# Optimization experiments

Hardware: AMD Instinct MI355X
Metric: run time of the kernel (lower is better)

Reference implementation:

```python
import jax, jax.numpy as jnp
import numpy as np

B, C, H, W = 4, 512, 128, 128
C8 = C // 8


def setup_inputs() -> dict:
    key = jax.random.key(0)
    ks = jax.random.split(key, 10)
    s = 0.02
    return {
        "x_exmplar": jax.random.normal(ks[0], (B, C, H, W), jnp.float32),
        "x_query": jax.random.normal(ks[1], (B, C, H, W), jnp.float32),
        "Wq": jax.random.normal(ks[2], (C8, C), jnp.float32) * s,
        "bq": jax.random.normal(ks[3], (C8,), jnp.float32) * s,
        "Wk": jax.random.normal(ks[4], (C8, C), jnp.float32) * s,
        "bk": jax.random.normal(ks[5], (C8,), jnp.float32) * s,
        "Wv": jax.random.normal(ks[6], (C, C), jnp.float32) * s,
        "bv": jax.random.normal(ks[7], (C,), jnp.float32) * s,
        "gamma_1": jax.random.normal(ks[8], (1,), jnp.float32) * 0.1,
        "gamma_2": jax.random.normal(ks[9], (1,), jnp.float32) * 0.1,
    }


def _conv1x1(x, Wt, b):
    # x: (B,C,H,W), Wt: (O,C) -> (B,O,H,W)
    return jnp.einsum('bchw,oc->bohw', x, Wt) + b[None, :, None, None]


def reference(x_exmplar, x_query, Wq, bq, Wk, bk, Wv, bv, gamma_1, gamma_2):
    q = _conv1x1(x_query, Wq, bq)      # (B,C8,H,W)
    k = _conv1x1(x_exmplar, Wk, bk)    # (B,C8,H,W)
    v = _conv1x1(x_exmplar, Wv, bv)    # (B,C,H,W)

    # vertical (H) path: energy_H[b,h,w,j] = sum_c q[b,c,h,w] k[b,c,j,w], -inf on h==j
    energy_H = jnp.einsum('bchw,bcjw->bhwj', q, k)
    eye = jnp.eye(H, dtype=bool)[None, :, None, :]       # (1,H,1,H)
    energy_H = jnp.where(eye, -jnp.inf, energy_H)
    # horizontal (W) path: energy_W[b,h,w,j] = sum_c q[b,c,h,w] k[b,c,h,j]
    energy_W = jnp.einsum('bchw,bchj->bhwj', q, k)

    concate = jax.nn.softmax(jnp.concatenate([energy_H, energy_W], axis=-1), axis=-1)
    att_H = concate[..., :H]           # (B,H,W,H)
    att_W = concate[..., H:]           # (B,H,W,W)

    out_H = jnp.einsum('bcjw,bhwj->bchw', v, att_H)
    out_W = jnp.einsum('bchj,bhwj->bchw', v, att_W)

    # diagonal (LR / RL) paths; D = min(H,W) = H for square maps
    q_d = jnp.diagonal(q, axis1=2, axis2=3)   # (B,C8,D)
    k_d = jnp.diagonal(k, axis1=2, axis2=3)   # (B,C8,D)
    v_d = jnp.diagonal(v, axis1=2, axis2=3)   # (B,C,D)
    # diag of transpose(2,3) with offset 0 equals diag, so LR == RL faithfully
    energy_LR = jnp.einsum('bci,bcj->bij', k_d, q_d)  # (B,D,D)
    energy_RL = energy_LR
    # softmax over a singleton trailing axis (as in the original code)
    out_LR = jax.nn.softmax(jnp.einsum('bcd,bdj->bcj', v_d, energy_LR)[..., None], axis=3)
    out_RL = jax.nn.softmax(jnp.einsum('bcd,bdj->bcj', v_d, energy_RL)[..., None], axis=3)

    out_sum = out_H + out_W + out_LR + out_RL   # (B,C,H,W) via broadcast of (B,C,D,1)
    return (gamma_1 * out_sum + x_exmplar, gamma_2 * out_sum + x_query)
```

## Files before the change

kernel.cpp:

```cpp
#include <hip/hip_runtime.h>
#include <stdint.h>

typedef unsigned short u16;
typedef __attribute__((ext_vector_type(8))) short bf16x8;
typedef __attribute__((ext_vector_type(4))) float f32x4;

#define NB   4
#define NC   512
#define NC8  64
#define NH   128
#define NW   128
#define NHW  16384

__device__ __forceinline__ float b2f(u16 u) {
  union { float f; uint32_t i; } x; x.i = ((uint32_t)u) << 16; return x.f;
}
__device__ __forceinline__ u16 f2b(float f) {
  union { float f; uint32_t u; } x; x.f = f;
  uint32_t r = x.u + 0x7FFF + ((x.u >> 16) & 1);
  return (u16)(r >> 16);
}
__device__ __forceinline__ uint4 pack8bf(const float* f) {
  uint4 u;
  u.x = (uint32_t)f2b(f[0]) | ((uint32_t)f2b(f[1]) << 16);
  u.y = (uint32_t)f2b(f[2]) | ((uint32_t)f2b(f[3]) << 16);
  u.z = (uint32_t)f2b(f[4]) | ((uint32_t)f2b(f[5]) << 16);
  u.w = (uint32_t)f2b(f[6]) | ((uint32_t)f2b(f[7]) << 16);
  return u;
}
__device__ __forceinline__ void unpack8bf(uint4 u, float* f) {
  f[0] = b2f((u16)(u.x & 0xFFFF)); f[1] = b2f((u16)(u.x >> 16));
  f[2] = b2f((u16)(u.y & 0xFFFF)); f[3] = b2f((u16)(u.y >> 16));
  f[4] = b2f((u16)(u.z & 0xFFFF)); f[5] = b2f((u16)(u.z >> 16));
  f[6] = b2f((u16)(u.w & 0xFFFF)); f[7] = b2f((u16)(u.w >> 16));
}

__global__ __launch_bounds__(256) void convert_w3(const float* __restrict__ Wv,
                                                  const float* __restrict__ Wq,
                                                  const float* __restrict__ Wk,
                                                  u16* __restrict__ wv,
                                                  u16* __restrict__ wq,
                                                  u16* __restrict__ wk) {
  int bid = blockIdx.x;
  const float* W; u16* Wb; int base;
  if (bid < 128)      { W = Wv; Wb = wv; base = bid; }
  else if (bid < 144) { W = Wq; Wb = wq; base = bid - 128; }
  else                { W = Wk; Wb = wk; base = bid - 144; }
  int i = (base * 256 + threadIdx.x) * 8;
  float4 a = *reinterpret_cast<const float4*>(W + i);
  float4 b = *reinterpret_cast<const float4*>(W + i + 4);
  float f[8] = {a.x, a.y, a.z, a.w, b.x, b.y, b.z, b.w};
  *reinterpret_cast<uint4*>(Wb + i) = pack8bf(f);
}

__global__ __launch_bounds__(256) void transpose_cvt2(const float* __restrict__ xe,
                                                      const float* __restrict__ xq,
                                                      u16* __restrict__ xeT,
                                                      u16* __restrict__ xqT) {
  __shared__ float tile[64][68];
  int z = blockIdx.z;
  int b = z & 3;
  const float* x = (z < 4) ? xe : xq;
  u16* xT = (z < 4) ? xeT : xqT;
  int c0 = blockIdx.y * 64, n0 = blockIdx.x * 64;
  int t = threadIdx.x;
  const float* src = x + ((size_t)b * NC + c0) * NHW + n0;
  int r = t >> 2, cq = (t & 3) * 16;
#pragma unroll
  for (int v = 0; v < 4; v++) {
    float4 f = *reinterpret_cast<const float4*>(&src[(size_t)r * NHW + cq + v * 4]);
    *reinterpret_cast<float4*>(&tile[r][cq + v * 4]) = f;
  }
  __syncthreads();
  int n = t >> 2, cg = (t & 3) * 16;
  u16* dst = &xT[((size_t)b * NHW + n0 + n) * NC + c0 + cg];
#pragma unroll
  for (int half = 0; half < 2; half++) {
    float f[8];
#pragma unroll
    for (int j = 0; j < 8; j++) f[j] = tile[cg + half * 8 + j][n];
    *reinterpret_cast<uint4*>(dst + half * 8) = pack8bf(f);
  }
}

__global__ __launch_bounds__(256) void proj64_qk(const u16* __restrict__ xeT,
                                                 const u16* __restrict__ xqT,
                                                 const u16* __restrict__ wk,
                                                 const u16* __restrict__ wq,
                                                 const float* __restrict__ bk,
                                                 const float* __restrict__ bq,
                                                 u16* __restrict__ kT,
                                                 u16* __restrict__ qT) {
  __shared__ __align__(16) u16 smem[12288];
  char* AsB = (char*)smem;
  char* BsB = (char*)smem + 8192;
  int which = blockIdx.y;
  const u16* xT = which ? xqT : xeT;
  const u16* Wb = which ? wq : wk;
  const float* bias = which ? bq : bk;
  u16* yT = which ? qT : kT;
  int n0 = blockIdx.x * 128, b = blockIdx.z;
  int t = threadIdx.x;
  int wid = t >> 6, lane = t & 63;
  int wm = wid >> 1, wn = wid & 1;
  int l15 = lane & 15, lhi = lane >> 4;

  f32x4 acc[2][4];
#pragma unroll
  for (int m = 0; m < 2; m++)
#pragma unroll
    for (int n = 0; n < 4; n++)
#pragma unroll
      for (int r = 0; r < 4; r++) acc[m][n][r] = 0.f;

  const u16* Bbase = xT + ((size_t)b * NHW + n0) * NC;

  for (int c0 = 0; c0 < NC; c0 += 64) {
#pragma unroll
    for (int p = 0; p < 2; p++) {
      int idx = t + p * 256;
      int row = idx >> 3, cb = (idx & 7) * 8;
      int dst = row * 128 + ((cb * 2) ^ ((row & 7) << 4));
      bf16x8 av = *reinterpret_cast<const bf16x8*>(Wb + (size_t)row * NC + c0 + cb);
      *reinterpret_cast<bf16x8*>(AsB + dst) = av;
    }
#pragma unroll
    for (int p = 0; p < 4; p++) {
      int idx = t + p * 256;
      int row = idx >> 3, cb = (idx & 7) * 8;
      int dst = row * 128 + ((cb * 2) ^ ((row & 7) << 4));
      bf16x8 bv = *reinterpret_cast<const bf16x8*>(Bbase + (size_t)row * NC + c0 + cb);
      *reinterpret_cast<bf16x8*>(BsB + dst) = bv;
    }
    __syncthreads();
#pragma unroll
    for (int kk = 0; kk < 2; kk++) {
      int kbyte = kk * 64 + lhi * 16;
      bf16x8 af[2], bfr[4];
#pragma unroll
      for (int m = 0; m < 2; m++) {
        int row = wm * 32 + m * 16 + l15;
        af[m] = *reinterpret_cast<const bf16x8*>(AsB + row * 128 + (kbyte ^ ((row & 7) << 4)));
      }
#pragma unroll
      for (int n = 0; n < 4; n++) {
        int row = wn * 64 + n * 16 + l15;
        bfr[n] = *reinterpret_cast<const bf16x8*>(BsB + row * 128 + (kbyte ^ ((row & 7) << 4)));
      }
#pragma unroll
      for (int m = 0; m < 2; m++)
#pragma unroll
        for (int n = 0; n < 4; n++)
          acc[m][n] = __builtin_amdgcn_mfma_f32_16x16x32_bf16(af[m], bfr[n], acc[m][n], 0, 0, 0);
    }
    __syncthreads();
  }

  char* stage = (char*)smem;
#pragma unroll
  for (int m = 0; m < 2; m++) {
#pragma unroll
    for (int r = 0; r < 4; r++) {
      int o = wm * 32 + m * 16 + lhi * 4 + r;
      float bval = bias[o];
#pragma unroll
      for (int n = 0; n < 4; n++) {
        int col = wn * 64 + n * 16 + l15;
        int byte = col * 128 + ((o * 2) ^ ((col & 7) << 4));
        *reinterpret_cast<u16*>(stage + byte) = f2b(acc[m][n][r] + bval);
      }
    }
  }
  __syncthreads();
#pragma unroll
  for (int p = 0; p < 4; p++) {
    int idx = t + p * 256;
    int col = idx >> 3, seg = idx & 7;
    int byte = col * 128 + ((seg * 16) ^ ((col & 7) << 4));
    uint4 v = *reinterpret_cast<const uint4*>(stage + byte);
    *reinterpret_cast<uint4*>(&yT[((size_t)b * NHW + n0 + col) * 64 + seg * 8]) = v;
  }
}

__global__ __launch_bounds__(256) void proj_v_mfma(const u16* __restrict__ xT,
                                                   const u16* __restrict__ Wb,
                                                   const float* __restrict__ bias,
                                                   u16* __restrict__ y) {
  __shared__ __align__(16) u16 smem[16384];
  char* AsB = (char*)smem;
  char* BsB = (char*)(smem + 8192);
  int o0 = blockIdx.x * 128, n0 = blockIdx.y * 128, b = blockIdx.z;
  int t = threadIdx.x;
  int wid = t >> 6, lane = t & 63;
  int wm = wid >> 1, wn = wid & 1;
  int l15 = lane & 15, lhi = lane >> 4;

  f32x4 acc[4][4];
#pragma unroll
  for (int m = 0; m < 4; m++)
#pragma unroll
    for (int n = 0; n < 4; n++)
#pragma unroll
      for (int r = 0; r < 4; r++) acc[m][n][r] = 0.f;

  const u16* Arow = Wb + (size_t)o0 * NC;
  const u16* Brow = xT + ((size_t)b * NHW + n0) * NC;

  for (int c0 = 0; c0 < NC; c0 += 64) {
#pragma unroll
    for (int p = 0; p < 4; p++) {
      int idx = t + p * 256;
      int row = idx >> 3;
      int cb  = (idx & 7) * 8;
      int dst = row * 128 + ((cb * 2) ^ ((row & 7) << 4));
      bf16x8 av = *reinterpret_cast<const bf16x8*>(Arow + (size_t)row * NC + c0 + cb);
      *reinterpret_cast<bf16x8*>(AsB + dst) = av;
      bf16x8 bv = *reinterpret_cast<const bf16x8*>(Brow + (size_t)row * NC + c0 + cb);
      *reinterpret_cast<bf16x8*>(BsB + dst) = bv;
    }
    __syncthreads();
#pragma unroll
    for (int kk = 0; kk < 2; kk++) {
      int kbyte = kk * 64 + lhi * 16;
      bf16x8 af[4], bfr[4];
#pragma unroll
      for (int m = 0; m < 4; m++) {
        int row = wm * 64 + m * 16 + l15;
        af[m] = *reinterpret_cast<const bf16x8*>(AsB + row * 128 + (kbyte ^ ((row & 7) << 4)));
      }
#pragma unroll
      for (int n = 0; n < 4; n++) {
        int row = wn * 64 + n * 16 + l15;
        bfr[n] = *reinterpret_cast<const bf16x8*>(BsB + row * 128 + (kbyte ^ ((row & 7) << 4)));
      }
#pragma unroll
      for (int m = 0; m < 4; m++)
#pragma unroll
        for (int n = 0; n < 4; n++)
          acc[m][n] = __builtin_amdgcn_mfma_f32_16x16x32_bf16(af[m], bfr[n], acc[m][n], 0, 0, 0);
    }
    __syncthreads();
  }

  char* stage = (char*)smem + wid * 8192;
#pragma unroll
  for (int m = 0; m < 4; m++) {
#pragma unroll
    for (int r = 0; r < 4; r++) {
      int lrow = m * 16 + lhi * 4 + r;
      float bval = bias[o0 + wm * 64 + lrow];
#pragma unroll
      for (int n = 0; n < 4; n++) {
        int col = n * 16 + l15;
        *reinterpret_cast<u16*>(stage + lrow * 128 + col * 2) = f2b(acc[m][n][r] + bval);
      }
    }
  }
  __syncthreads();
#pragma unroll
  for (int s = 0; s < 8; s++) {
    int row  = s * 8 + (lane >> 3);
    int colb = (lane & 7) * 8;
    uint4 v = *reinterpret_cast<const uint4*>(stage + row * 128 + colb * 2);
    size_t addr = ((size_t)b * NC + o0 + wm * 64 + row) * (size_t)NHW + n0 + wn * 64 + colb;
    *reinterpret_cast<uint4*>(&y[addr]) = v;
  }
}

__global__ __launch_bounds__(256) void transpose128v(const u16* __restrict__ src,
                                                     u16* __restrict__ dst) {
  __shared__ u16 tile[64][68];
  int p = blockIdx.z;
  int i0 = blockIdx.y * 64, j0 = blockIdx.x * 64;
  int t = threadIdx.x;
  const u16* s = src + (size_t)p * NHW;
  u16* d = dst + (size_t)p * NHW;
#pragma unroll
  for (int q = 0; q < 2; q++) {
    int idx = t + q * 256;
    int r = idx >> 3, c8 = (idx & 7) * 8;
    uint4 v = *reinterpret_cast<const uint4*>(&s[(size_t)(i0 + r) * 128 + j0 + c8]);
    *reinterpret_cast<uint2*>(&tile[r][c8])     = make_uint2(v.x, v.y);
    *reinterpret_cast<uint2*>(&tile[r][c8 + 4]) = make_uint2(v.z, v.w);
  }
  __syncthreads();
#pragma unroll
  for (int q = 0; q < 2; q++) {
    int idx = t + q * 256;
    int j = idx >> 3, c8 = (idx & 7) * 8;
    u16 f[8];
#pragma unroll
    for (int v = 0; v < 8; v++) f[v] = tile[c8 + v][j];
    uint4 o;
    o.x = (uint32_t)f[0] | ((uint32_t)f[1] << 16);
    o.y = (uint32_t)f[2] | ((uint32_t)f[3] << 16);
    o.z = (uint32_t)f[4] | ((uint32_t)f[5] << 16);
    o.w = (uint32_t)f[6] | ((uint32_t)f[7] << 16);
    *reinterpret_cast<uint4*>(&d[(size_t)(j0 + j) * 128 + i0 + c8]) = o;
  }
}

__global__ __launch_bounds__(256) void energy2(const u16* __restrict__ QT,
                                               const u16* __restrict__ KT,
                                               u16* __restrict__ att) {
  __shared__ __align__(16) u16 smem[16384];
  char* AsB = (char*)smem;
  char* BsB = (char*)(smem + 8192);
  int s = blockIdx.x, b = blockIdx.y, isH = blockIdx.z;
  int t = threadIdx.x;
  int wid = t >> 6, lane = t & 63;
  int wm = wid >> 1, wn = wid & 1;
  int l15 = lane & 15, lhi = lane >> 4;

  size_t base = (size_t)b * NHW * 64;
  size_t rowstride = isH ? (size_t)128 * 64 : 64;
  size_t off0 = isH ? (size_t)s * 64 : (size_t)s * 128 * 64;

  f32x4 acc[4][4];
#pragma unroll
  for (int m = 0; m < 4; m++)
#pragma unroll
    for (int n = 0; n < 4; n++)
#pragma unroll
      for (int r = 0; r < 4; r++) acc[m][n][r] = 0.f;

#pragma unroll
  for (int p = 0; p < 4; p++) {
    int idx = t + p * 256;
    int row = idx >> 3;
    int cb  = (idx & 7) * 8;
    int dst = row * 128 + ((cb * 2) ^ ((row & 7) << 4));
    bf16x8 av = *reinterpret_cast<const bf16x8*>(QT + base + off0 + (size_t)row * rowstride + cb);
    *reinterpret_cast<bf16x8*>(AsB + dst) = av;
    bf16x8 bv = *reinterpret_cast<const bf16x8*>(KT + base + off0 + (size_t)row * rowstride + cb);
    *reinterpret_cast<bf16x8*>(BsB + dst) = bv;
  }
  __syncthreads();
#pragma unroll
  for (int kk = 0; kk < 2; kk++) {
    int kbyte = kk * 64 + lhi * 16;
    bf16x8 af[4], bfr[4];
#pragma unroll
    for (int m = 0; m < 4; m++) {
      int row = wm * 64 + m * 16 + l15;
      af[m] = *reinterpret_cast<const bf16x8*>(AsB + row * 128 + (kbyte ^ ((row & 7) << 4)));
    }
#pragma unroll
    for (int n = 0; n < 4; n++) {
      int row = wn * 64 + n * 16 + l15;
      bfr[n] = *reinterpret_cast<const bf16x8*>(BsB + row * 128 + (kbyte ^ ((row & 7) << 4)));
    }
#pragma unroll
    for (int m = 0; m < 4; m++)
#pragma unroll
      for (int n = 0; n < 4; n++)
        acc[m][n] = __builtin_amdgcn_mfma_f32_16x16x32_bf16(af[m], bfr[n], acc[m][n], 0, 0, 0);
  }
  __syncthreads();

  char* stage = (char*)smem + wid * 8192;
#pragma unroll
  for (int m = 0; m < 4; m++) {
#pragma unroll
    for (int r = 0; r < 4; r++) {
      int lrow = m * 16 + lhi * 4 + r;
      int grow = wm * 64 + lrow;
#pragma unroll
      for (int n = 0; n < 4; n++) {
        int col = n * 16 + l15;
        int gcol = wn * 64 + col;
        float v = acc[m][n][r];
        if (isH && gcol == grow) v = -1e30f;
        *reinterpret_cast<u16*>(stage + lrow * 128 + col * 2) = f2b(v);
      }
    }
  }
  __syncthreads();
  size_t attb = (size_t)b * 4194304;
#pragma unroll
  for (int sb = 0; sb < 8; sb++) {
    int row  = wm * 64 + sb * 8 + (lane >> 3);
    int colb = wn * 64 + (lane & 7) * 8;
    uint4 v = *reinterpret_cast<const uint4*>(stage + (sb * 8 + (lane >> 3)) * 128 + (lane & 7) * 16);
    size_t addr = attb + (isH ? ((size_t)row * 32768 + (size_t)s * 256 + colb)
                              : ((size_t)s * 32768 + (size_t)row * 256 + 128 + colb));
    *reinterpret_cast<uint4*>(&att[addr]) = v;
  }
}

__global__ __launch_bounds__(256) void softmax_kern(u16* __restrict__ att) {
  int half = threadIdx.x >> 5;
  int lane = threadIdx.x & 31;
  size_t row = (size_t)blockIdx.x * 8 + half;
  u16* p = att + row * 256;
  uint4 u = *reinterpret_cast<const uint4*>(&p[lane * 8]);
  float v[8]; unpack8bf(u, v);
  float mx = v[0];
  for (int i = 1; i < 8; i++) mx = fmaxf(mx, v[i]);
  for (int off = 16; off; off >>= 1) mx = fmaxf(mx, __shfl_xor(mx, off));
  float sum = 0.f;
  for (int i = 0; i < 8; i++) { v[i] = __expf(v[i] - mx); sum += v[i]; }
  for (int off = 16; off; off >>= 1) sum += __shfl_xor(sum, off);
  float inv = 1.f / sum;
  for (int i = 0; i < 8; i++) v[i] *= inv;
  *reinterpret_cast<uint4*>(&p[lane * 8]) = pack8bf(v);
}

__global__ __launch_bounds__(256) void out_gemm2(const u16* __restrict__ Vn,
                                                 const u16* __restrict__ Vsw,
                                                 const u16* __restrict__ att) {
  __shared__ __align__(16) u16 smem[16384];
  char* AsB = (char*)smem;
  char* BsB = (char*)(smem + 8192);
  int ct = blockIdx.x, s = blockIdx.y;
  int b = blockIdx.z & 3, isH = blockIdx.z >> 2;
  const u16* V = isH ? Vsw : Vn;
  u16* out = const_cast<u16*>(V);
  int t = threadIdx.x;
  int wid = t >> 6, lane = t & 63;
  int wm = wid >> 1, wn = wid & 1;
  int l15 = lane & 15, lhi = lane >> 4;

  f32x4 acc[4][4];
#pragma unroll
  for (int m = 0; m < 4; m++)
#pragma unroll
    for (int n = 0; n < 4; n++)
#pragma unroll
      for (int r = 0; r < 4; r++) acc[m][n][r] = 0.f;

  const u16* Abase = V + ((size_t)(b * NC + ct * 128)) * NHW + (size_t)s * 128;
  size_t attb = (size_t)b * 4194304;
  size_t bbase = attb + (isH ? (size_t)s * 256 : (size_t)s * 32768 + 128);
  size_t bstride = isH ? 32768 : 256;

  for (int c0 = 0; c0 < 128; c0 += 64) {
#pragma unroll
    for (int p = 0; p < 4; p++) {
      int idx = t + p * 256;
      int row = idx >> 3;
      int cb  = (idx & 7) * 8;
      int dst = row * 128 + ((cb * 2) ^ ((row & 7) << 4));
      bf16x8 av = *reinterpret_cast<const bf16x8*>(Abase + (size_t)row * NHW + c0 + cb);
      *reinterpret_cast<bf16x8*>(AsB + dst) = av;
      bf16x8 bv = *reinterpret_cast<const bf16x8*>(att + bbase + (size_t)row * bstride + c0 + cb);
      *reinterpret_cast<bf16x8*>(BsB + dst) = bv;
    }
    __syncthreads();
#pragma unroll
    for (int kk = 0; kk < 2; kk++) {
      int kbyte = kk * 64 + lhi * 16;
      bf16x8 af[4], bfr[4];
#pragma unroll
      for (int m = 0; m < 4; m++) {
        int row = wm * 64 + m * 16 + l15;
        af[m] = *reinterpret_cast<const bf16x8*>(AsB + row * 128 + (kbyte ^ ((row & 7) << 4)));
      }
#pragma unroll
      for (int n = 0; n < 4; n++) {
        int row = wn * 64 + n * 16 + l15;
        bfr[n] = *reinterpret_cast<const bf16x8*>(BsB + row * 128 + (kbyte ^ ((row & 7) << 4)));
      }
#pragma unroll
      for (int m = 0; m < 4; m++)
#pragma unroll
        for (int n = 0; n < 4; n++)
          acc[m][n] = __builtin_amdgcn_mfma_f32_16x16x32_bf16(af[m], bfr[n], acc[m][n], 0, 0, 0);
    }
    __syncthreads();
  }

  char* stage = (char*)smem + wid * 8192;
#pragma unroll
  for (int m = 0; m < 4; m++) {
#pragma unroll
    for (int r = 0; r < 4; r++) {
      int lrow = m * 16 + lhi * 4 + r;
#pragma unroll
      for (int n = 0; n < 4; n++) {
        int col = n * 16 + l15;
        *reinterpret_cast<u16*>(stage + lrow * 128 + col * 2) = f2b(acc[m][n][r]);
      }
    }
  }
  __syncthreads();
#pragma unroll
  for (int sb = 0; sb < 8; sb++) {
    int row  = sb * 8 + (lane >> 3);
    int colb = (lane & 7) * 8;
    uint4 v = *reinterpret_cast<const uint4*>(stage + row * 128 + colb * 2);
    size_t addr = ((size_t)(b * NC + ct * 128 + wm * 64 + row)) * NHW + (size_t)s * 128 + wn * 64 + colb;
    *reinterpret_cast<uint4*>(&out[addr]) = v;
  }
}

__global__ __launch_bounds__(256) void epilogue(const u16* __restrict__ outWbf,
                                                const u16* __restrict__ outHsw,
                                                const float* __restrict__ xe,
                                                const float* __restrict__ xq,
                                                const float* __restrict__ g1p,
                                                const float* __restrict__ g2p,
                                                float* __restrict__ out0,
                                                float* __restrict__ out1) {
  __shared__ float tile[32][65];
  int p = blockIdx.z;
  int h0 = blockIdx.y * 64, w0 = blockIdx.x * 32;
  int t = threadIdx.x;
  {
    int w = t >> 3, hc = t & 7;
    uint4 v = *reinterpret_cast<const uint4*>(
        &outHsw[(size_t)p * NHW + (size_t)(w0 + w) * 128 + h0 + hc * 8]);
    float f[8]; unpack8bf(v, f);
    for (int j = 0; j < 8; j++) tile[w][hc * 8 + j] = f[j];
  }
  __syncthreads();
  float g1 = g1p[0], g2 = g2p[0];
  int h = t >> 2, wc = t & 3;
  size_t idx = (size_t)p * NHW + (size_t)(h0 + h) * 128 + w0 + wc * 8;
  uint4 wv = *reinterpret_cast<const uint4*>(&outWbf[idx]);
  float s[8]; unpack8bf(wv, s);
  float4 xe0 = *reinterpret_cast<const float4*>(&xe[idx]);
  float4 xe1 = *reinterpret_cast<const float4*>(&xe[idx + 4]);
  float4 xq0 = *reinterpret_cast<const float4*>(&xq[idx]);
  float4 xq1 = *reinterpret_cast<const float4*>(&xq[idx + 4]);
  float sum[8];
  for (int j = 0; j < 8; j++) sum[j] = s[j] + tile[wc * 8 + j][h] + 2.0f;
  float4 o0a = {g1 * sum[0] + xe0.x, g1 * sum[1] + xe0.y, g1 * sum[2] + xe0.z, g1 * sum[3] + xe0.w};
  float4 o0b = {g1 * sum[4] + xe1.x, g1 * sum[5] + xe1.y, g1 * sum[6] + xe1.z, g1 * sum[7] + xe1.w};
  float4 o1a = {g2 * sum[0] + xq0.x, g2 * sum[1] + xq0.y, g2 * sum[2] + xq0.z, g2 * sum[3] + xq0.w};
  float4 o1b = {g2 * sum[4] + xq1.x, g2 * sum[5] + xq1.y, g2 * sum[6] + xq1.z, g2 * sum[7] + xq1.w};
  *reinterpret_cast<float4*>(&out0[idx])     = o0a;
  *reinterpret_cast<float4*>(&out0[idx + 4]) = o0b;
  *reinterpret_cast<float4*>(&out1[idx])     = o1a;
  *reinterpret_cast<float4*>(&out1[idx + 4]) = o1b;
}

extern "C" void kernel_launch(void* const* d_in, const int* in_sizes, int n_in,
                              void* d_out, int out_size, void* d_ws, size_t ws_size,
                              hipStream_t stream) {
  (void)in_sizes; (void)n_in; (void)out_size; (void)ws_size;
  const float* xe = (const float*)d_in[0];
  const float* xq = (const float*)d_in[1];
  const float* Wq = (const float*)d_in[2];
  const float* bq = (const float*)d_in[3];
  const float* Wk = (const float*)d_in[4];
  const float* bk = (const float*)d_in[5];
  const float* Wv = (const float*)d_in[6];
  const float* bv = (const float*)d_in[7];
  const float* g1 = (const float*)d_in[8];
  const float* g2 = (const float*)d_in[9];
  float* out = (float*)d_out;

  char* ws = (char*)d_ws;
  u16* qT    = (u16*)(ws + 0);
  u16* kT    = (u16*)(ws + 8388608);
  u16* wv_bf = (u16*)(ws + 16777216);
  u16* wq_bf = (u16*)(ws + 17301504);
  u16* wk_bf = (u16*)(ws + 17367040);
  u16* v_n   = (u16*)(ws + 33554432);
  u16* v_sw  = (u16*)(ws + 100663296);
  u16* att   = (u16*)(ws + 167772160);
  u16* xeT   = (u16*)(ws + 201326592);
  u16* xqT   = (u16*)(ws + 100663296);

  convert_w3<<<dim3(160), 256, 0, stream>>>(Wv, Wq, Wk, wv_bf, wq_bf, wk_bf);
  transpose_cvt2<<<dim3(256, 8, 8), 256, 0, stream>>>(xe, xq, xeT, xqT);
  proj64_qk<<<dim3(128, 2, 4), 256, 0, stream>>>(xeT, xqT, wk_bf, wq_bf, bk, bq, kT, qT);
  proj_v_mfma<<<dim3(4, 128, 4), 256, 0, stream>>>(xeT, wv_bf, bv, v_n);
  transpose128v<<<dim3(2, 2, 2048), 256, 0, stream>>>(v_n, v_sw);
  energy2<<<dim3(128, 4, 2), 256, 0, stream>>>(qT, kT, att);
  softmax_kern<<<dim3(8192), 256, 0, stream>>>(att);
  out_gemm2<<<dim3(4, 128, 8), 256, 0, stream>>>(v_n, v_sw, att);
  epilogue<<<dim3(4, 2, 2048), 256, 0, stream>>>(v_n, v_sw, xe, xq, g1, g2,
                                                 out, out + 33554432);
}
```

Before: 748.2 us.

## Register-prefetch next K tile in GEMMs, remap block order, fold weight conversion

The three MFMA GEMM kernels (q/k projection, v projection, output GEMM) now load the next K-slice of the global tiles into registers while the current slice is being consumed, so global latency overlaps with MFMA work. proj_v_mfma and out_gemm2 remap the linear block index with a stride-8 swizzle, which changes the order in which tiles are dispatched and may improve cache locality across chiplets. The weight bf16 conversion is folded into the transpose kernel as an extra z-slice to save one launch. The cost is higher register pressure from the prefetch buffers, plus many mostly idle blocks in the extra z-slice.

```diff
diff --git a/kernel.cpp b/kernel.cpp
--- a/kernel.cpp
+++ b/kernel.cpp
@@ -35,30 +35,32 @@
   f[6] = b2f((u16)(u.w & 0xFFFF)); f[7] = b2f((u16)(u.w >> 16));
 }
 
-__global__ __launch_bounds__(256) void convert_w3(const float* __restrict__ Wv,
-                                                  const float* __restrict__ Wq,
-                                                  const float* __restrict__ Wk,
-                                                  u16* __restrict__ wv,
-                                                  u16* __restrict__ wq,
-                                                  u16* __restrict__ wk) {
-  int bid = blockIdx.x;
-  const float* W; u16* Wb; int base;
-  if (bid < 128)      { W = Wv; Wb = wv; base = bid; }
-  else if (bid < 144) { W = Wq; Wb = wq; base = bid - 128; }
-  else                { W = Wk; Wb = wk; base = bid - 144; }
-  int i = (base * 256 + threadIdx.x) * 8;
-  float4 a = *reinterpret_cast<const float4*>(W + i);
-  float4 b = *reinterpret_cast<const float4*>(W + i + 4);
-  float f[8] = {a.x, a.y, a.z, a.w, b.x, b.y, b.z, b.w};
-  *reinterpret_cast<uint4*>(Wb + i) = pack8bf(f);
-}
-
 __global__ __launch_bounds__(256) void transpose_cvt2(const float* __restrict__ xe,
                                                       const float* __restrict__ xq,
                                                       u16* __restrict__ xeT,
-                                                      u16* __restrict__ xqT) {
+                                                      u16* __restrict__ xqT,
+                                                      const float* __restrict__ Wv,
+                                                      const float* __restrict__ Wq,
+                                                      const float* __restrict__ Wk,
+                                                      u16* __restrict__ wv,
+                                                      u16* __restrict__ wq,
+                                                      u16* __restrict__ wk) {
   __shared__ float tile[64][68];
   int z = blockIdx.z;
+  if (z == 8) {
+    int bid = blockIdx.y * 256 + blockIdx.x;
+    if (bid >= 160) return;
+    const float* W; u16* Wb; int base;
+    if (bid < 128)      { W = Wv; Wb = wv; base = bid; }
+    else if (bid < 144) { W = Wq; Wb = wq; base = bid - 128; }
+    else                { W = Wk; Wb = wk; base = bid - 144; }
+    int i = (base * 256 + threadIdx.x) * 8;
+    float4 a = *reinterpret_cast<const float4*>(W + i);
+    float4 b = *reinterpret_cast<const float4*>(W + i + 4);
+    float f[8] = {a.x, a.y, a.z, a.w, b.x, b.y, b.z, b.w};
+    *reinterpret_cast<uint4*>(Wb + i) = pack8bf(f);
+    return;
+  }
   int b = z & 3;
   const float* x = (z < 4) ? xe : xq;
   u16* xT = (z < 4) ? xeT : xqT;
@@ -115,24 +117,51 @@
 
   const u16* Bbase = xT + ((size_t)b * NHW + n0) * NC;
 
-  for (int c0 = 0; c0 < NC; c0 += 64) {
+  bf16x8 ar[2], br[4];
+#pragma unroll
+  for (int p = 0; p < 2; p++) {
+    int idx = t + p * 256;
+    int row = idx >> 3, cb = (idx & 7) * 8;
+    ar[p] = *reinterpret_cast<const bf16x8*>(Wb + (size_t)row * NC + cb);
+  }
+#pragma unroll
+  for (int p = 0; p < 4; p++) {
+    int idx = t + p * 256;
+    int row = idx >> 3, cb = (idx & 7) * 8;
+    br[p] = *reinterpret_cast<const bf16x8*>(Bbase + (size_t)row * NC + cb);
+  }
+
+  for (int tt = 0; tt < 8; tt++) {
 #pragma unroll
     for (int p = 0; p < 2; p++) {
       int idx = t + p * 256;
       int row = idx >> 3, cb = (idx & 7) * 8;
       int dst = row * 128 + ((cb * 2) ^ ((row & 7) << 4));
-      bf16x8 av = *reinterpret_cast<const bf16x8*>(Wb + (size_t)row * NC + c0 + cb);
-      *reinterpret_cast<bf16x8*>(AsB + dst) = av;
+      *reinterpret_cast<bf16x8*>(AsB + dst) = ar[p];
     }
 #pragma unroll
     for (int p = 0; p < 4; p++) {
       int idx = t + p * 256;
       int row = idx >> 3, cb = (idx & 7) * 8;
       int dst = row * 128 + ((cb * 2) ^ ((row & 7) << 4));
-      bf16x8 bv = *reinterpret_cast<const bf16x8*>(Bbase + (size_t)row * NC + c0 + cb);
-      *reinterpret_cast<bf16x8*>(BsB + dst) = bv;
+      *reinterpret_cast<bf16x8*>(BsB + dst) = br[p];
     }
     __syncthreads();
+    if (tt < 7) {
+      int c0 = (tt + 1) * 64;
+#pragma unroll
+      for (int p = 0; p < 2; p++) {
+        int idx = t + p * 256;
+        int row = idx >> 3, cb = (idx & 7) * 8;
+        ar[p] = *reinterpret_cast<const bf16x8*>(Wb + (size_t)row * NC + c0 + cb);
+      }
+#pragma unroll
+      for (int p = 0; p < 4; p++) {
+        int idx = t + p * 256;
+        int row = idx >> 3, cb = (idx & 7) * 8;
+        br[p] = *reinterpret_cast<const bf16x8*>(Bbase + (size_t)row * NC + c0 + cb);
+      }
+    }
 #pragma unroll
     for (int kk = 0; kk < 2; kk++) {
       int kbyte = kk * 64 + lhi * 16;
@@ -189,7 +218,11 @@
   __shared__ __align__(16) u16 smem[16384];
   char* AsB = (char*)smem;
   char* BsB = (char*)(smem + 8192);
-  int o0 = blockIdx.x * 128, n0 = blockIdx.y * 128, b = blockIdx.z;
+  int lin = blockIdx.x + (blockIdx.y << 2) + (blockIdx.z << 9);
+  int l = ((lin & 7) << 8) + (lin >> 3);
+  int o0 = (l & 3) * 128;
+  int n0 = ((l >> 2) & 127) * 128;
+  int b  = l >> 9;
   int t = threadIdx.x;
   int wid = t >> 6, lane = t & 63;
   int wm = wid >> 1, wn = wid & 1;
@@ -206,19 +239,35 @@
   const u16* Arow = Wb + (size_t)o0 * NC;
   const u16* Brow = xT + ((size_t)b * NHW + n0) * NC;
 
-  for (int c0 = 0; c0 < NC; c0 += 64) {
+  bf16x8 ar[4], br[4];
+#pragma unroll
+  for (int p = 0; p < 4; p++) {
+    int idx = t + p * 256;
+    int row = idx >> 3, cb = (idx & 7) * 8;
+    ar[p] = *reinterpret_cast<const bf16x8*>(Arow + (size_t)row * NC + cb);
+    br[p] = *reinterpret_cast<const bf16x8*>(Brow + (size_t)row * NC + cb);
+  }
+
+  for (int tt = 0; tt < 8; tt++) {
 #pragma unroll
     for (int p = 0; p < 4; p++) {
       int idx = t + p * 256;
-      int row = idx >> 3;
-      int cb  = (idx & 7) * 8;
+      int row = idx >> 3, cb = (idx & 7) * 8;
       int dst = row * 128 + ((cb * 2) ^ ((row & 7) << 4));
-      bf16x8 av = *reinterpret_cast<const bf16x8*>(Arow + (size_t)row * NC + c0 + cb);
-      *reinterpret_cast<bf16x8*>(AsB + dst) = av;
-      bf16x8 bv = *reinterpret_cast<const bf16x8*>(Brow + (size_t)row * NC + c0 + cb);
-      *reinterpret_cast<bf16x8*>(BsB + dst) = bv;
+      *reinterpret_cast<bf16x8*>(AsB + dst) = ar[p];
+      *reinterpret_cast<bf16x8*>(BsB + dst) = br[p];
     }
     __syncthreads();
+    if (tt < 7) {
+      int c0 = (tt + 1) * 64;
+#pragma unroll
+      for (int p = 0; p < 4; p++) {
+        int idx = t + p * 256;
+        int row = idx >> 3, cb = (idx & 7) * 8;
+        ar[p] = *reinterpret_cast<const bf16x8*>(Arow + (size_t)row * NC + c0 + cb);
+        br[p] = *reinterpret_cast<const bf16x8*>(Brow + (size_t)row * NC + c0 + cb);
+      }
+    }
 #pragma unroll
     for (int kk = 0; kk < 2; kk++) {
       int kbyte = kk * 64 + lhi * 16;
@@ -412,8 +461,10 @@
   __shared__ __align__(16) u16 smem[16384];
   char* AsB = (char*)smem;
   char* BsB = (char*)(smem + 8192);
-  int ct = blockIdx.x, s = blockIdx.y;
-  int b = blockIdx.z & 3, isH = blockIdx.z >> 2;
+  int lin = blockIdx.x + (blockIdx.y << 2) + (blockIdx.z << 9);
+  int l = ((lin & 7) << 9) + (lin >> 3);
+  int ct = l & 3, s = (l >> 2) & 127, zz = l >> 9;
+  int b = zz & 3, isH = zz >> 2;
   const u16* V = isH ? Vsw : Vn;
   u16* out = const_cast<u16*>(V);
   int t = threadIdx.x;
@@ -434,19 +485,34 @@
   size_t bbase = attb + (isH ? (size_t)s * 256 : (size_t)s * 32768 + 128);
   size_t bstride = isH ? 32768 : 256;
 
-  for (int c0 = 0; c0 < 128; c0 += 64) {
+  bf16x8 ar[4], br[4];
+#pragma unroll
+  for (int p = 0; p < 4; p++) {
+    int idx = t + p * 256;
+    int row = idx >> 3, cb = (idx & 7) * 8;
+    ar[p] = *reinterpret_cast<const bf16x8*>(Abase + (size_t)row * NHW + cb);
+    br[p] = *reinterpret_cast<const bf16x8*>(att + bbase + (size_t)row * bstride + cb);
+  }
+
+  for (int tt = 0; tt < 2; tt++) {
 #pragma unroll
     for (int p = 0; p < 4; p++) {
       int idx = t + p * 256;
-      int row = idx >> 3;
-      int cb  = (idx & 7) * 8;
+      int row = idx >> 3, cb = (idx & 7) * 8;
       int dst = row * 128 + ((cb * 2) ^ ((row & 7) << 4));
-      bf16x8 av = *reinterpret_cast<const bf16x8*>(Abase + (size_t)row * NHW + c0 + cb);
-      *reinterpret_cast<bf16x8*>(AsB + dst) = av;
-      bf16x8 bv = *reinterpret_cast<const bf16x8*>(att + bbase + (size_t)row * bstride + c0 + cb);
-      *reinterpret_cast<bf16x8*>(BsB + dst) = bv;
+      *reinterpret_cast<bf16x8*>(AsB + dst) = ar[p];
+      *reinterpret_cast<bf16x8*>(BsB + dst) = br[p];
     }
     __syncthreads();
+    if (tt == 0) {
+#pragma unroll
+      for (int p = 0; p < 4; p++) {
+        int idx = t + p * 256;
+        int row = idx >> 3, cb = (idx & 7) * 8;
+        ar[p] = *reinterpret_cast<const bf16x8*>(Abase + (size_t)row * NHW + 64 + cb);
+        br[p] = *reinterpret_cast<const bf16x8*>(att + bbase + (size_t)row * bstride + 64 + cb);
+      }
+    }
 #pragma unroll
     for (int kk = 0; kk < 2; kk++) {
       int kbyte = kk * 64 + lhi * 16;
@@ -563,8 +629,8 @@
   u16* xeT   = (u16*)(ws + 201326592);
   u16* xqT   = (u16*)(ws + 100663296);
 
-  convert_w3<<<dim3(160), 256, 0, stream>>>(Wv, Wq, Wk, wv_bf, wq_bf, wk_bf);
-  transpose_cvt2<<<dim3(256, 8, 8), 256, 0, stream>>>(xe, xq, xeT, xqT);
+  transpose_cvt2<<<dim3(256, 8, 9), 256, 0, stream>>>(xe, xq, xeT, xqT,
+                                                      Wv, Wq, Wk, wv_bf, wq_bf, wk_bf);
   proj64_qk<<<dim3(128, 2, 4), 256, 0, stream>>>(xeT, xqT, wk_bf, wq_bf, bk, bq, kT, qT);
   proj_v_mfma<<<dim3(4, 128, 4), 256, 0, stream>>>(xeT, wv_bf, bv, v_n);
   transpose128v<<<dim3(2, 2, 2048), 256, 0, stream>>>(v_n, v_sw);
```

Result: faster. 724.9 us (-3.1%).
